# Performance work log

Measured on AMD Instinct MI355X. Metric: run time of the kernel, lower is better.

## Reference

```python
import jax, jax.numpy as jnp
import numpy as np

B, L, D, A = 4, 4096, 256, 64  # batch, seq_len, n_embd, att_size

def setup_inputs() -> dict:
    key = jax.random.key(0)
    kx, kq, kk, kv = jax.random.split(key, 4)
    x = jax.random.normal(kx, (B, L, D), dtype=jnp.float32)
    # torch nn.Linear(n_embd, att_size) weight is [att_size, n_embd]; we store transposed [D, A]
    s = 1.0 / np.sqrt(D)
    Wq = jax.random.normal(kq, (D, A), dtype=jnp.float32) * s
    Wk = jax.random.normal(kk, (D, A), dtype=jnp.float32) * s
    Wv = jax.random.normal(kv, (D, A), dtype=jnp.float32) * s
    return {"x": x, "Wq": Wq, "Wk": Wk, "Wv": Wv}

def reference(x, Wq, Wk, Wv):
    # q,k,v: [B,L,A]
    q = jnp.einsum('bld,da->bla', x, Wq)
    k = jnp.einsum('bld,da->bla', x, Wk)
    v = jnp.einsum('bld,da->bla', x, Wv)
    # NOTE: original module does NOT scale by 1/sqrt(att_size)
    scores = jnp.einsum('bqa,bka->bqk', q, k)  # [B,L,L]
    Lq = x.shape[1]
    causal = jnp.tril(jnp.ones((Lq, Lq), dtype=bool))
    scores = jnp.where(causal, scores, -jnp.inf)
    weights = jax.nn.softmax(scores, axis=-1)
    # dropout is identity in eval mode
    out = jnp.einsum('bqk,bka->bqa', weights, v)  # [B,L,A]
    return out
```

## Files before the change

### kernel.cpp

```cpp
#include <hip/hip_runtime.h>
#include <math.h>

#define B_ 4
#define L_ 4096
#define D_ 256
#define A_ 64
#define M_ (B_*L_)

typedef _Float16 half4 __attribute__((ext_vector_type(4)));
typedef _Float16 half8 __attribute__((ext_vector_type(8)));
typedef __attribute__((ext_vector_type(4))) float floatx4;

__device__ __forceinline__ unsigned short f2h_(float f) {
    _Float16 h = (_Float16)f;
    return __builtin_bit_cast(unsigned short, h);
}

__global__ __launch_bounds__(256) void wconv_kernel(
    const float* __restrict__ Wq, const float* __restrict__ Wk,
    const float* __restrict__ Wv, unsigned short* __restrict__ wt)
{
    const int w = blockIdx.x, t = threadIdx.x;
    const float* W = (w == 0) ? Wq : (w == 1) ? Wk : Wv;
    unsigned short* o = wt + w * A_ * D_;
    const float scale = (w == 0) ? 1.44269504f : 1.0f;
    __shared__ float T[A_ * 260];
    #pragma unroll
    for (int p = 0; p < 16; ++p) {
        int idx = p * 256 + t;
        int d = idx >> 4, a4 = (idx & 15) * 4;
        float4 v = *(const float4*)(W + d * A_ + a4);
        T[(a4 + 0) * 260 + d] = v.x * scale;
        T[(a4 + 1) * 260 + d] = v.y * scale;
        T[(a4 + 2) * 260 + d] = v.z * scale;
        T[(a4 + 3) * 260 + d] = v.w * scale;
    }
    __syncthreads();
    const int a = t >> 2, d0 = (t & 3) * 64;
    #pragma unroll
    for (int i = 0; i < 16; ++i) {
        float4 v = *(const float4*)(&T[a * 260 + d0 + 4 * i]);
        ushort4 s;
        s.x = f2h_(v.x); s.y = f2h_(v.y); s.z = f2h_(v.z); s.w = f2h_(v.w);
        *(ushort4*)(o + a * D_ + d0 + 4 * i) = s;
    }
}

__global__ __launch_bounds__(384) void proj_kernel(
    const float* __restrict__ x,
    const unsigned short* __restrict__ wt,
    unsigned short* __restrict__ qo,
    unsigned short* __restrict__ ko,
    unsigned short* __restrict__ vto)
{
    __shared__ __align__(16) unsigned short Xh[32 * 264];
    __shared__ __align__(16) unsigned short Cst[6 * 1536];
    const int t = threadIdx.x, m0 = blockIdx.x * 32;

    #pragma unroll
    for (int p = 0; p < 6; ++p) {
        int idx = p * 384 + t;
        if (idx < 2048) {
            int row = idx >> 6, col = (idx & 63) * 4;
            float4 v = *(const float4*)(x + (size_t)(m0 + row) * D_ + col);
            ushort4 s;
            s.x = f2h_(v.x); s.y = f2h_(v.y); s.z = f2h_(v.z); s.w = f2h_(v.w);
            *(ushort4*)(Xh + row * 264 + col) = s;
        }
    }
    __syncthreads();

    const int wid = t >> 6, lane = t & 63, c = lane & 15, g = lane >> 4;
    const int w = wid >> 1, mt = wid & 1;

    half8 xa[8];
    #pragma unroll
    for (int s = 0; s < 8; ++s)
        xa[s] = *(const half8*)(Xh + (16 * mt + c) * 264 + 32 * s + 8 * g);

    const unsigned short* wsrc = wt + w * A_ * D_;
    unsigned short* Cw = Cst + wid * 1536;
    #pragma unroll
    for (int nt = 0; nt < 4; ++nt) {
        floatx4 acc = {0.f, 0.f, 0.f, 0.f};
        #pragma unroll
        for (int s = 0; s < 8; ++s) {
            half8 wb = *(const half8*)(wsrc + (16 * nt + c) * D_ + 32 * s + 8 * g);
            acc = __builtin_amdgcn_mfma_f32_16x16x32_f16(xa[s], wb, acc, 0, 0, 0);
        }
        if (w < 2) {
            #pragma unroll
            for (int r = 0; r < 4; ++r)
                Cw[(4 * g + r) * 72 + 16 * nt + c] = f2h_(acc[r]);
        } else {
            #pragma unroll
            for (int r = 0; r < 4; ++r)
                Cw[(16 * nt + c) * 24 + 4 * g + r] = f2h_(acc[r]);
        }
    }

    if (w < 2) {
        unsigned short* o = (w == 0) ? qo : ko;
        const int row16 = lane >> 2, seg = lane & 3;
        uint4 d0 = *(const uint4*)(Cw + row16 * 72 + seg * 16);
        uint4 d1 = *(const uint4*)(Cw + row16 * 72 + seg * 16 + 8);
        unsigned short* p = o + (size_t)(m0 + 16 * mt + row16) * A_ + seg * 16;
        *(uint4*)(p) = d0;
        *(uint4*)(p + 8) = d1;
    }
    __syncthreads();
    if (t < 256) {
        const int a = t >> 2, quarter = t & 3;
        const int o = quarter * 8, mtv = o >> 4, idx = o & 15;
        uint4 d = *(const uint4*)(Cst + (4 + mtv) * 1536 + a * 24 + idx);
        const int bb = m0 >> 12, l0 = m0 & (L_ - 1);
        *(uint4*)(vto + ((size_t)(bb * A_ + a)) * L_ + l0 + o) = d;
    }
}

__global__ __launch_bounds__(256) void attn_kernel(
    const unsigned short* __restrict__ qb,
    const unsigned short* __restrict__ kb,
    const unsigned short* __restrict__ vt,
    float* __restrict__ out,
    float* __restrict__ po1,
    float2* __restrict__ ml0,
    float2* __restrict__ ml1)
{
    __shared__ __align__(16) unsigned short smem[4 * 4608];
    unsigned short* Ks = smem;
    unsigned short* Vs = smem + 2 * 4608;

    const int t    = threadIdx.x;
    const int lane = t & 63;
    const int wid  = t >> 6;
    const int qsub = wid >> 1;
    const int ph   = wid & 1;
    const int c    = lane & 15;
    const int g    = lane >> 4;
    const int b    = blockIdx.y;
    const int bx   = blockIdx.x;
    const int qt   = 127 - (bx >> 1);
    const int h    = bx & 1;
    const int q0   = qt * 32;
    const int qrow0 = q0 + 16 * qsub;
    const int qme  = qrow0 + c;

    const size_t base  = (size_t)b * L_ * A_;
    const size_t vbase = (size_t)b * A_ * L_;

    half8 qf[2];
    {
        const unsigned short* qp = qb + base + (size_t)(qrow0 + c) * A_ + g * 8;
        qf[0] = *(const half8*)(qp);
        qf[1] = *(const half8*)(qp + 32);
    }

    floatx4 O4[4];
    #pragma unroll
    for (int at = 0; at < 4; ++at) O4[at] = (floatx4){0.f, 0.f, 0.f, 0.f};
    float m_ = -INFINITY, l_ = 0.f;

    const int T   = (q0 >> 6) + 1;
    const int Th  = (T + 1) >> 1;
    const int t0  = h ? Th : 0;
    const int t1  = h ? T : Th;
    const int nIt = (t1 - t0 + 1) >> 1;
    const int Tm1 = T - 1;

    for (int it = 0; it < nIt; ++it) {
        __syncthreads();
        #pragma unroll
        for (int tile = 0; tile < 2; ++tile) {
            const int kts = t0 + 2 * it + tile;
            if (kts < t1) {
                const int k0s = kts << 6;
                #pragma unroll
                for (int i = 0; i < 2; ++i) {
                    const int cid = t + (i << 8);
                    const int row = cid >> 3, c8 = cid & 7;
                    uint4 dK = *(const uint4*)(kb + base + (size_t)k0s * 64 + cid * 8);
                    *(uint4*)(Ks + tile * 4608 + row * 72 + c8 * 8) = dK;
                    uint4 dV = *(const uint4*)(vt + vbase + (size_t)row * L_ + k0s + c8 * 8);
                    *(uint4*)(Vs + tile * 4608 + row * 72 + c8 * 8) = dV;
                }
            }
        }
        __syncthreads();

        const int kt = t0 + 2 * it + ph;
        if (kt >= t1) continue;
        const int k0 = kt << 6;
        const unsigned short* Kw = Ks + ph * 4608;
        const unsigned short* Vw = Vs + ph * 4608;

        floatx4 S4[4];
        #pragma unroll
        for (int nt = 0; nt < 4; ++nt) S4[nt] = (floatx4){0.f, 0.f, 0.f, 0.f};
        #pragma unroll
        for (int s = 0; s < 2; ++s)
            #pragma unroll
            for (int nt = 0; nt < 4; ++nt) {
                half8 kf = *(const half8*)(Kw + (16 * nt + c) * 72 + 32 * s + 8 * g);
                S4[nt] = __builtin_amdgcn_mfma_f32_16x16x32_f16(kf, qf[s], S4[nt], 0, 0, 0);
            }

        if (kt == Tm1) {
            #pragma unroll
            for (int nt = 0; nt < 4; ++nt)
                #pragma unroll
                for (int r = 0; r < 4; ++r)
                    if (k0 + 16 * nt + 4 * g + r > qme) S4[nt][r] = -INFINITY;
        }

        float tm = fmaxf(fmaxf(fmaxf(S4[0][0], S4[0][1]), fmaxf(S4[0][2], S4[0][3])),
                         fmaxf(fmaxf(S4[1][0], S4[1][1]), fmaxf(S4[1][2], S4[1][3])));
        tm = fmaxf(tm, fmaxf(fmaxf(fmaxf(S4[2][0], S4[2][1]), fmaxf(S4[2][2], S4[2][3])),
                             fmaxf(fmaxf(S4[3][0], S4[3][1]), fmaxf(S4[3][2], S4[3][3]))));
        tm = fmaxf(tm, __shfl_xor(tm, 16));
        tm = fmaxf(tm, __shfl_xor(tm, 32));
        const float mn  = fmaxf(m_, tm);
        const float mnc = fmaxf(mn, -3.0e38f);
        const float al  = exp2f(fminf(m_ - mnc, 0.f));
        float rs = 0.f;
        half4 pf[4];
        #pragma unroll
        for (int nt = 0; nt < 4; ++nt) {
            #pragma unroll
            for (int r = 0; r < 4; ++r) {
                float p = exp2f(S4[nt][r] - mnc);
                S4[nt][r] = p;
                rs += p;
            }
            pf[nt][0] = (_Float16)S4[nt][0];
            pf[nt][1] = (_Float16)S4[nt][1];
            pf[nt][2] = (_Float16)S4[nt][2];
            pf[nt][3] = (_Float16)S4[nt][3];
        }
        rs += __shfl_xor(rs, 16);
        rs += __shfl_xor(rs, 32);
        l_ = l_ * al + rs;
        m_ = mn;

        #pragma unroll
        for (int at = 0; at < 4; ++at) {
            O4[at] *= al;
            #pragma unroll
            for (int nt = 0; nt < 4; ++nt) {
                half4 va = *(const half4*)(Vw + (16 * at + c) * 72 + 16 * nt + 4 * g);
                O4[at] = __builtin_amdgcn_mfma_f32_16x16x16f16(va, pf[nt], O4[at], 0, 0, 0);
            }
        }
    }

    __syncthreads();
    float*  Of  = (float*)smem;
    float2* mlb = (float2*)(smem + 8192);
    #pragma unroll
    for (int at = 0; at < 4; ++at) {
        float4 v; v.x = O4[at][0]; v.y = O4[at][1]; v.z = O4[at][2]; v.w = O4[at][3];
        ((float4*)Of)[wid * 256 + at * 64 + lane] = v;
    }
    if (g == 0) { float2 ml; ml.x = m_; ml.y = l_; mlb[wid * 16 + c] = ml; }
    __syncthreads();

    {
        const int q32 = t >> 3, seg = t & 7;
        const int qs = q32 >> 4, cc = q32 & 15;
        const float2 A0 = mlb[(2 * qs) * 16 + cc];
        const float2 A1 = mlb[(2 * qs + 1) * 16 + cc];
        const float mf = fmaxf(A0.x, A1.x);
        const float mc = fmaxf(mf, -3.0e38f);
        const float w0 = exp2f(A0.x - mc);
        const float w1 = exp2f(A1.x - mc);
        const float ls = w0 * A0.y + w1 * A1.y;
        float res[8];
        #pragma unroll
        for (int u = 0; u < 8; ++u) {
            const int a = seg * 8 + u;
            const int at = a >> 4, gg = (a >> 2) & 3, r = a & 3;
            const int i0 = ((2 * qs) * 256 + at * 64 + gg * 16 + cc) * 4 + r;
            const int i1 = ((2 * qs + 1) * 256 + at * 64 + gg * 16 + cc) * 4 + r;
            res[u] = w0 * Of[i0] + w1 * Of[i1];
        }
        float* PO = h ? po1 : out;
        float* p = PO + (base + (size_t)(q0 + q32) * A_) + seg * 8;
        *(float4*)(p)     = make_float4(res[0], res[1], res[2], res[3]);
        *(float4*)(p + 4) = make_float4(res[4], res[5], res[6], res[7]);
        if (seg == 0) {
            float2 ml; ml.x = mf; ml.y = ls;
            (h ? ml1 : ml0)[b * L_ + q0 + q32] = ml;
        }
    }
}

__global__ __launch_bounds__(256) void merge_kernel(
    float* __restrict__ out, const float* __restrict__ po1,
    const float2* __restrict__ ml0, const float2* __restrict__ ml1)
{
    const int tg = blockIdx.x * 256 + threadIdx.x;
    const int q = tg >> 4;
    const float2 a0 = ml0[q], a1 = ml1[q];
    const float mf = fmaxf(a0.x, a1.x);
    const float mc = fmaxf(mf, -3.0e38f);
    const float w0 = exp2f(a0.x - mc);
    const float w1 = exp2f(a1.x - mc);
    const float inv = 1.f / (w0 * a0.y + w1 * a1.y);
    float4 o0 = ((const float4*)out)[tg];
    float4 o1 = ((const float4*)po1)[tg];
    float4 r;
    r.x = (o0.x * w0 + o1.x * w1) * inv;
    r.y = (o0.y * w0 + o1.y * w1) * inv;
    r.z = (o0.z * w0 + o1.z * w1) * inv;
    r.w = (o0.w * w0 + o1.w * w1) * inv;
    ((float4*)out)[tg] = r;
}

extern "C" void kernel_launch(void* const* d_in, const int* in_sizes, int n_in,
                              void* d_out, int out_size, void* d_ws, size_t ws_size,
                              hipStream_t stream) {
    const float* x  = (const float*)d_in[0];
    const float* Wq = (const float*)d_in[1];
    const float* Wk = (const float*)d_in[2];
    const float* Wv = (const float*)d_in[3];

    char* ws = (char*)d_ws;
    unsigned short* qb = (unsigned short*)(ws);
    unsigned short* kb = (unsigned short*)(ws + (2u << 20));
    unsigned short* vt = (unsigned short*)(ws + (4u << 20));
    unsigned short* wt = (unsigned short*)(ws + (6u << 20));
    float*  po1 = (float*) (ws + (6u << 20) + 98304);
    float2* ml0 = (float2*)(ws + (6u << 20) + 98304 + (4u << 20));
    float2* ml1 = (float2*)(ws + (6u << 20) + 98304 + (4u << 20) + 131072);
    float* out = (float*)d_out;

    hipLaunchKernelGGL(wconv_kernel, dim3(3), dim3(256), 0, stream, Wq, Wk, Wv, wt);
    hipLaunchKernelGGL(proj_kernel, dim3(M_ / 32), dim3(384), 0, stream, x, wt, qb, kb, vt);
    hipLaunchKernelGGL(attn_kernel, dim3(256, B_), dim3(256), 0, stream,
                       qb, kb, vt, out, po1, ml0, ml1);
    hipLaunchKernelGGL(merge_kernel, dim3(1024), dim3(256), 0, stream, out, po1, ml0, ml1);
}
```

Baseline: 138.1 us.

## Restructure attention into 8-wave blocks with paired q-tiles and fused split-K merge

The attention kernel now runs 512 threads per block, with four waves splitting key tiles for each 16-row query group. Each block processes a heavy and a light causal query tile (127-bx and bx) to balance load. The combine across waves happens in shared memory, which removes the separate merge kernel and the partial-output buffers in the workspace. K tiles are prefetched into registers and written to LDS after a barrier. V fragments are loaded straight from global memory into registers with one tile of lookahead instead of being staged in LDS. The grid shrinks to 256 blocks, and the heavier per-thread V register use may limit occupancy.

After: 198.2 us. 1.44x slower.

```diff
diff --git a/kernel.cpp b/kernel.cpp
--- a/kernel.cpp
+++ b/kernel.cpp
@@ -118,202 +118,199 @@
     }
 }
 
-__global__ __launch_bounds__(256) void attn_kernel(
+__global__ __launch_bounds__(512, 2) void attn_kernel(
     const unsigned short* __restrict__ qb,
     const unsigned short* __restrict__ kb,
     const unsigned short* __restrict__ vt,
-    float* __restrict__ out,
-    float* __restrict__ po1,
-    float2* __restrict__ ml0,
-    float2* __restrict__ ml1)
+    float* __restrict__ out)
 {
     __shared__ __align__(16) unsigned short smem[4 * 4608];
-    unsigned short* Ks = smem;
-    unsigned short* Vs = smem + 2 * 4608;
 
     const int t    = threadIdx.x;
     const int lane = t & 63;
     const int wid  = t >> 6;
-    const int qsub = wid >> 1;
-    const int ph   = wid & 1;
+    const int qsub = wid >> 2;
+    const int ph   = wid & 3;
     const int c    = lane & 15;
     const int g    = lane >> 4;
     const int b    = blockIdx.y;
     const int bx   = blockIdx.x;
-    const int qt   = 127 - (bx >> 1);
-    const int h    = bx & 1;
-    const int q0   = qt * 32;
-    const int qrow0 = q0 + 16 * qsub;
-    const int qme  = qrow0 + c;
 
     const size_t base  = (size_t)b * L_ * A_;
     const size_t vbase = (size_t)b * A_ * L_;
 
-    half8 qf[2];
-    {
-        const unsigned short* qp = qb + base + (size_t)(qrow0 + c) * A_ + g * 8;
-        qf[0] = *(const half8*)(qp);
-        qf[1] = *(const half8*)(qp + 32);
-    }
-
-    floatx4 O4[4];
-    #pragma unroll
-    for (int at = 0; at < 4; ++at) O4[at] = (floatx4){0.f, 0.f, 0.f, 0.f};
-    float m_ = -INFINITY, l_ = 0.f;
-
-    const int T   = (q0 >> 6) + 1;
-    const int Th  = (T + 1) >> 1;
-    const int t0  = h ? Th : 0;
-    const int t1  = h ? T : Th;
-    const int nIt = (t1 - t0 + 1) >> 1;
-    const int Tm1 = T - 1;
-
-    for (int it = 0; it < nIt; ++it) {
+    const int srow = t >> 3, sc8 = t & 7;
+
+    for (int p = 0; p < 2; ++p) {
+        const int qt = (p == 0) ? (127 - bx) : bx;
+        const int q0 = qt * 32;
+        const int qrow0 = q0 + 16 * qsub;
+        const int qme = qrow0 + c;
+        const int T = (qt >> 1) + 1;
+        const int nR = (T + 3) >> 2;
+
+        half8 qf[2];
+        {
+            const unsigned short* qp = qb + base + (size_t)(qrow0 + c) * A_ + g * 8;
+            qf[0] = *(const half8*)(qp);
+            qf[1] = *(const half8*)(qp + 32);
+        }
+
+        floatx4 O4[4];
+        #pragma unroll
+        for (int at = 0; at < 4; ++at) O4[at] = (floatx4){0.f, 0.f, 0.f, 0.f};
+        float m_ = -INFINITY, l_ = 0.f;
+
         __syncthreads();
         #pragma unroll
-        for (int tile = 0; tile < 2; ++tile) {
-            const int kts = t0 + 2 * it + tile;
-            if (kts < t1) {
-                const int k0s = kts << 6;
-                #pragma unroll
-                for (int i = 0; i < 2; ++i) {
-                    const int cid = t + (i << 8);
-                    const int row = cid >> 3, c8 = cid & 7;
-                    uint4 dK = *(const uint4*)(kb + base + (size_t)k0s * 64 + cid * 8);
-                    *(uint4*)(Ks + tile * 4608 + row * 72 + c8 * 8) = dK;
-                    uint4 dV = *(const uint4*)(vt + vbase + (size_t)row * L_ + k0s + c8 * 8);
-                    *(uint4*)(Vs + tile * 4608 + row * 72 + c8 * 8) = dV;
-                }
-            }
-        }
-        __syncthreads();
-
-        const int kt = t0 + 2 * it + ph;
-        if (kt >= t1) continue;
-        const int k0 = kt << 6;
-        const unsigned short* Kw = Ks + ph * 4608;
-        const unsigned short* Vw = Vs + ph * 4608;
-
-        floatx4 S4[4];
-        #pragma unroll
-        for (int nt = 0; nt < 4; ++nt) S4[nt] = (floatx4){0.f, 0.f, 0.f, 0.f};
-        #pragma unroll
-        for (int s = 0; s < 2; ++s)
+        for (int u = 0; u < 4; ++u) {
+            if (u < T) {
+                uint4 dK = *(const uint4*)(kb + base + ((size_t)(u << 6) * 64 + t * 8));
+                *(uint4*)(smem + u * 4608 + srow * 72 + sc8 * 8) = dK;
+            }
+        }
+        half4 vc[4][4], vn[4][4];
+        if (ph < T) {
+            const unsigned short* vp = vt + vbase + (ph << 6);
             #pragma unroll
-            for (int nt = 0; nt < 4; ++nt) {
-                half8 kf = *(const half8*)(Kw + (16 * nt + c) * 72 + 32 * s + 8 * g);
-                S4[nt] = __builtin_amdgcn_mfma_f32_16x16x32_f16(kf, qf[s], S4[nt], 0, 0, 0);
-            }
-
-        if (kt == Tm1) {
-            #pragma unroll
-            for (int nt = 0; nt < 4; ++nt)
-                #pragma unroll
-                for (int r = 0; r < 4; ++r)
-                    if (k0 + 16 * nt + 4 * g + r > qme) S4[nt][r] = -INFINITY;
-        }
-
-        float tm = fmaxf(fmaxf(fmaxf(S4[0][0], S4[0][1]), fmaxf(S4[0][2], S4[0][3])),
-                         fmaxf(fmaxf(S4[1][0], S4[1][1]), fmaxf(S4[1][2], S4[1][3])));
-        tm = fmaxf(tm, fmaxf(fmaxf(fmaxf(S4[2][0], S4[2][1]), fmaxf(S4[2][2], S4[2][3])),
-                             fmaxf(fmaxf(S4[3][0], S4[3][1]), fmaxf(S4[3][2], S4[3][3]))));
-        tm = fmaxf(tm, __shfl_xor(tm, 16));
-        tm = fmaxf(tm, __shfl_xor(tm, 32));
-        const float mn  = fmaxf(m_, tm);
-        const float mnc = fmaxf(mn, -3.0e38f);
-        const float al  = exp2f(fminf(m_ - mnc, 0.f));
-        float rs = 0.f;
-        half4 pf[4];
-        #pragma unroll
-        for (int nt = 0; nt < 4; ++nt) {
-            #pragma unroll
-            for (int r = 0; r < 4; ++r) {
-                float p = exp2f(S4[nt][r] - mnc);
-                S4[nt][r] = p;
-                rs += p;
-            }
-            pf[nt][0] = (_Float16)S4[nt][0];
-            pf[nt][1] = (_Float16)S4[nt][1];
-            pf[nt][2] = (_Float16)S4[nt][2];
-            pf[nt][3] = (_Float16)S4[nt][3];
-        }
-        rs += __shfl_xor(rs, 16);
-        rs += __shfl_xor(rs, 32);
-        l_ = l_ * al + rs;
-        m_ = mn;
-
+            for (int at = 0; at < 4; ++at)
+                #pragma unroll
+                for (int nt = 0; nt < 4; ++nt)
+                    vc[at][nt] = *(const half4*)(vp + (size_t)(16 * at + c) * L_ + 16 * nt + 4 * g);
+        }
+
+        for (int it = 0; it < nR; ++it) {
+            __syncthreads();
+            const int kt = 4 * it + ph;
+            const bool pfk = (it + 1 < nR);
+            uint4 nK[4];
+            if (pfk) {
+                #pragma unroll
+                for (int u = 0; u < 4; ++u) {
+                    const int kts = 4 * (it + 1) + u;
+                    if (kts < T)
+                        nK[u] = *(const uint4*)(kb + base + ((size_t)(kts << 6) * 64 + t * 8));
+                }
+            }
+            if (kt + 4 < T) {
+                const unsigned short* vp = vt + vbase + ((kt + 4) << 6);
+                #pragma unroll
+                for (int at = 0; at < 4; ++at)
+                    #pragma unroll
+                    for (int nt = 0; nt < 4; ++nt)
+                        vn[at][nt] = *(const half4*)(vp + (size_t)(16 * at + c) * L_ + 16 * nt + 4 * g);
+            }
+
+            if (kt < T) {
+                const int k0 = kt << 6;
+                const unsigned short* Kw = smem + ph * 4608;
+
+                floatx4 S4[4];
+                #pragma unroll
+                for (int nt = 0; nt < 4; ++nt) S4[nt] = (floatx4){0.f, 0.f, 0.f, 0.f};
+                #pragma unroll
+                for (int s = 0; s < 2; ++s)
+                    #pragma unroll
+                    for (int nt = 0; nt < 4; ++nt) {
+                        half8 kf = *(const half8*)(Kw + (16 * nt + c) * 72 + 32 * s + 8 * g);
+                        S4[nt] = __builtin_amdgcn_mfma_f32_16x16x32_f16(kf, qf[s], S4[nt], 0, 0, 0);
+                    }
+
+                if (kt == T - 1) {
+                    #pragma unroll
+                    for (int nt = 0; nt < 4; ++nt)
+                        #pragma unroll
+                        for (int r = 0; r < 4; ++r)
+                            if (k0 + 16 * nt + 4 * g + r > qme) S4[nt][r] = -INFINITY;
+                }
+
+                float tm = fmaxf(fmaxf(fmaxf(S4[0][0], S4[0][1]), fmaxf(S4[0][2], S4[0][3])),
+                                 fmaxf(fmaxf(S4[1][0], S4[1][1]), fmaxf(S4[1][2], S4[1][3])));
+                tm = fmaxf(tm, fmaxf(fmaxf(fmaxf(S4[2][0], S4[2][1]), fmaxf(S4[2][2], S4[2][3])),
+                                     fmaxf(fmaxf(S4[3][0], S4[3][1]), fmaxf(S4[3][2], S4[3][3]))));
+                tm = fmaxf(tm, __shfl_xor(tm, 16));
+                tm = fmaxf(tm, __shfl_xor(tm, 32));
+                const float mn  = fmaxf(m_, tm);
+                const float mnc = fmaxf(mn, -3.0e38f);
+                const float al  = exp2f(fminf(m_ - mnc, 0.f));
+                float rs = 0.f;
+                half4 pfr[4];
+                #pragma unroll
+                for (int nt = 0; nt < 4; ++nt) {
+                    #pragma unroll
+                    for (int r = 0; r < 4; ++r) {
+                        float pv = exp2f(S4[nt][r] - mnc);
+                        S4[nt][r] = pv;
+                        rs += pv;
+                    }
+                    pfr[nt][0] = (_Float16)S4[nt][0];
+                    pfr[nt][1] = (_Float16)S4[nt][1];
+                    pfr[nt][2] = (_Float16)S4[nt][2];
+                    pfr[nt][3] = (_Float16)S4[nt][3];
+                }
+                rs += __shfl_xor(rs, 16);
+                rs += __shfl_xor(rs, 32);
+                l_ = l_ * al + rs;
+                m_ = mn;
+
+                #pragma unroll
+                for (int at = 0; at < 4; ++at) {
+                    O4[at] *= al;
+                    #pragma unroll
+                    for (int nt = 0; nt < 4; ++nt)
+                        O4[at] = __builtin_amdgcn_mfma_f32_16x16x16f16(vc[at][nt], pfr[nt], O4[at], 0, 0, 0);
+                }
+                if (kt + 4 < T) {
+                    #pragma unroll
+                    for (int at = 0; at < 4; ++at)
+                        #pragma unroll
+                        for (int nt = 0; nt < 4; ++nt)
+                            vc[at][nt] = vn[at][nt];
+                }
+            }
+
+            __syncthreads();
+            if (pfk) {
+                #pragma unroll
+                for (int u = 0; u < 4; ++u)
+                    if (4 * (it + 1) + u < T)
+                        *(uint4*)(smem + u * 4608 + srow * 72 + sc8 * 8) = nK[u];
+            }
+        }
+
+        float4* Obuf = (float4*)smem;
+        float2* mlq  = (float2*)((char*)smem + 32768);
         #pragma unroll
         for (int at = 0; at < 4; ++at) {
-            O4[at] *= al;
-            #pragma unroll
-            for (int nt = 0; nt < 4; ++nt) {
-                half4 va = *(const half4*)(Vw + (16 * at + c) * 72 + 16 * nt + 4 * g);
-                O4[at] = __builtin_amdgcn_mfma_f32_16x16x16f16(va, pf[nt], O4[at], 0, 0, 0);
-            }
-        }
-    }
-
-    __syncthreads();
-    float*  Of  = (float*)smem;
-    float2* mlb = (float2*)(smem + 8192);
-    #pragma unroll
-    for (int at = 0; at < 4; ++at) {
-        float4 v; v.x = O4[at][0]; v.y = O4[at][1]; v.z = O4[at][2]; v.w = O4[at][3];
-        ((float4*)Of)[wid * 256 + at * 64 + lane] = v;
-    }
-    if (g == 0) { float2 ml; ml.x = m_; ml.y = l_; mlb[wid * 16 + c] = ml; }
-    __syncthreads();
-
-    {
-        const int q32 = t >> 3, seg = t & 7;
-        const int qs = q32 >> 4, cc = q32 & 15;
-        const float2 A0 = mlb[(2 * qs) * 16 + cc];
-        const float2 A1 = mlb[(2 * qs + 1) * 16 + cc];
-        const float mf = fmaxf(A0.x, A1.x);
-        const float mc = fmaxf(mf, -3.0e38f);
-        const float w0 = exp2f(A0.x - mc);
-        const float w1 = exp2f(A1.x - mc);
-        const float ls = w0 * A0.y + w1 * A1.y;
-        float res[8];
-        #pragma unroll
-        for (int u = 0; u < 8; ++u) {
-            const int a = seg * 8 + u;
-            const int at = a >> 4, gg = (a >> 2) & 3, r = a & 3;
-            const int i0 = ((2 * qs) * 256 + at * 64 + gg * 16 + cc) * 4 + r;
-            const int i1 = ((2 * qs + 1) * 256 + at * 64 + gg * 16 + cc) * 4 + r;
-            res[u] = w0 * Of[i0] + w1 * Of[i1];
-        }
-        float* PO = h ? po1 : out;
-        float* p = PO + (base + (size_t)(q0 + q32) * A_) + seg * 8;
-        *(float4*)(p)     = make_float4(res[0], res[1], res[2], res[3]);
-        *(float4*)(p + 4) = make_float4(res[4], res[5], res[6], res[7]);
-        if (seg == 0) {
-            float2 ml; ml.x = mf; ml.y = ls;
-            (h ? ml1 : ml0)[b * L_ + q0 + q32] = ml;
-        }
-    }
-}
-
-__global__ __launch_bounds__(256) void merge_kernel(
-    float* __restrict__ out, const float* __restrict__ po1,
-    const float2* __restrict__ ml0, const float2* __restrict__ ml1)
-{
-    const int tg = blockIdx.x * 256 + threadIdx.x;
-    const int q = tg >> 4;
-    const float2 a0 = ml0[q], a1 = ml1[q];
-    const float mf = fmaxf(a0.x, a1.x);
-    const float mc = fmaxf(mf, -3.0e38f);
-    const float w0 = exp2f(a0.x - mc);
-    const float w1 = exp2f(a1.x - mc);
-    const float inv = 1.f / (w0 * a0.y + w1 * a1.y);
-    float4 o0 = ((const float4*)out)[tg];
-    float4 o1 = ((const float4*)po1)[tg];
-    float4 r;
-    r.x = (o0.x * w0 + o1.x * w1) * inv;
-    r.y = (o0.y * w0 + o1.y * w1) * inv;
-    r.z = (o0.z * w0 + o1.z * w1) * inv;
-    r.w = (o0.w * w0 + o1.w * w1) * inv;
-    ((float4*)out)[tg] = r;
+            float4 v; v.x = O4[at][0]; v.y = O4[at][1]; v.z = O4[at][2]; v.w = O4[at][3];
+            Obuf[wid * 256 + at * 64 + lane] = v;
+        }
+        if (g == 0) { float2 ml; ml.x = m_; ml.y = l_; mlq[wid * 16 + c] = ml; }
+        __syncthreads();
+        {
+            const int q = t >> 4, seg = t & 15;
+            const int qs = q >> 4, cc = q & 15;
+            const int at = seg >> 2, gg = seg & 3;
+            const float2 A0 = mlq[(qs * 4 + 0) * 16 + cc];
+            const float2 A1 = mlq[(qs * 4 + 1) * 16 + cc];
+            const float2 A2 = mlq[(qs * 4 + 2) * 16 + cc];
+            const float2 A3 = mlq[(qs * 4 + 3) * 16 + cc];
+            const float mf = fmaxf(fmaxf(A0.x, A1.x), fmaxf(A2.x, A3.x));
+            const float w0 = exp2f(A0.x - mf), w1 = exp2f(A1.x - mf);
+            const float w2 = exp2f(A2.x - mf), w3 = exp2f(A3.x - mf);
+            const float inv = 1.f / (w0 * A0.y + w1 * A1.y + w2 * A2.y + w3 * A3.y);
+            const float4 o0 = Obuf[(qs * 4 + 0) * 256 + at * 64 + gg * 16 + cc];
+            const float4 o1 = Obuf[(qs * 4 + 1) * 256 + at * 64 + gg * 16 + cc];
+            const float4 o2 = Obuf[(qs * 4 + 2) * 256 + at * 64 + gg * 16 + cc];
+            const float4 o3 = Obuf[(qs * 4 + 3) * 256 + at * 64 + gg * 16 + cc];
+            float4 r;
+            r.x = (o0.x * w0 + o1.x * w1 + o2.x * w2 + o3.x * w3) * inv;
+            r.y = (o0.y * w0 + o1.y * w1 + o2.y * w2 + o3.y * w3) * inv;
+            r.z = (o0.z * w0 + o1.z * w1 + o2.z * w2 + o3.z * w3) * inv;
+            r.w = (o0.w * w0 + o1.w * w1 + o2.w * w2 + o3.w * w3) * inv;
+            *(float4*)(out + base + (size_t)(q0 + q) * A_ + seg * 4) = r;
+        }
+    }
 }
 
 extern "C" void kernel_launch(void* const* d_in, const int* in_sizes, int n_in,
@@ -329,14 +326,9 @@
     unsigned short* kb = (unsigned short*)(ws + (2u << 20));
     unsigned short* vt = (unsigned short*)(ws + (4u << 20));
     unsigned short* wt = (unsigned short*)(ws + (6u << 20));
-    float*  po1 = (float*) (ws + (6u << 20) + 98304);
-    float2* ml0 = (float2*)(ws + (6u << 20) + 98304 + (4u << 20));
-    float2* ml1 = (float2*)(ws + (6u << 20) + 98304 + (4u << 20) + 131072);
     float* out = (float*)d_out;
 
     hipLaunchKernelGGL(wconv_kernel, dim3(3), dim3(256), 0, stream, Wq, Wk, Wv, wt);
     hipLaunchKernelGGL(proj_kernel, dim3(M_ / 32), dim3(384), 0, stream, x, wt, qb, kb, vt);
-    hipLaunchKernelGGL(attn_kernel, dim3(256, B_), dim3(256), 0, stream,
-                       qb, kb, vt, out, po1, ml0, ml1);
-    hipLaunchKernelGGL(merge_kernel, dim3(1024), dim3(256), 0, stream, out, po1, ml0, ml1);
-}
+    hipLaunchKernelGGL(attn_kernel, dim3(64, B_), dim3(512), 0, stream, qb, kb, vt, out);
+}
```

## Have each attention wave process both query subtiles to reuse K/V fragments

Applied to the files above, without the earlier changes.

The attention block shrinks from four waves to two, and each wave now handles both 16-row query subtiles of the 32-row tile. Each K and V fragment read from LDS then feeds two MFMAs, which halves LDS read traffic per unit of compute and cuts the number of waves sharing the staged tiles. In exchange, per-wave register use roughly doubles (two sets of accumulators and scores), fewer threads share the global-to-LDS copy, and there are fewer waves available to hide latency. The in-block combine and the workspace offsets are adjusted to match.

New measurement: 141.9 us. 1.03x slower.

```diff
diff --git a/kernel.cpp b/kernel.cpp
--- a/kernel.cpp
+++ b/kernel.cpp
@@ -118,7 +118,7 @@
     }
 }
 
-__global__ __launch_bounds__(256) void attn_kernel(
+__global__ __launch_bounds__(128) void attn_kernel(
     const unsigned short* __restrict__ qb,
     const unsigned short* __restrict__ kb,
     const unsigned short* __restrict__ vt,
@@ -133,9 +133,7 @@
 
     const int t    = threadIdx.x;
     const int lane = t & 63;
-    const int wid  = t >> 6;
-    const int qsub = wid >> 1;
-    const int ph   = wid & 1;
+    const int ph   = t >> 6;
     const int c    = lane & 15;
     const int g    = lane >> 4;
     const int b    = blockIdx.y;
@@ -143,25 +141,28 @@
     const int qt   = 127 - (bx >> 1);
     const int h    = bx & 1;
     const int q0   = qt * 32;
-    const int qrow0 = q0 + 16 * qsub;
-    const int qme  = qrow0 + c;
 
     const size_t base  = (size_t)b * L_ * A_;
     const size_t vbase = (size_t)b * A_ * L_;
 
-    half8 qf[2];
-    {
-        const unsigned short* qp = qb + base + (size_t)(qrow0 + c) * A_ + g * 8;
-        qf[0] = *(const half8*)(qp);
-        qf[1] = *(const half8*)(qp + 32);
-    }
-
-    floatx4 O4[4];
-    #pragma unroll
-    for (int at = 0; at < 4; ++at) O4[at] = (floatx4){0.f, 0.f, 0.f, 0.f};
-    float m_ = -INFINITY, l_ = 0.f;
-
-    const int T   = (q0 >> 6) + 1;
+    half8 qf[2][2];
+    #pragma unroll
+    for (int u = 0; u < 2; ++u) {
+        const unsigned short* qp = qb + base + (size_t)(q0 + 16 * u + c) * A_ + g * 8;
+        qf[u][0] = *(const half8*)(qp);
+        qf[u][1] = *(const half8*)(qp + 32);
+    }
+
+    floatx4 O4[2][4];
+    float m_[2], l_[2];
+    #pragma unroll
+    for (int u = 0; u < 2; ++u) {
+        #pragma unroll
+        for (int at = 0; at < 4; ++at) O4[u][at] = (floatx4){0.f, 0.f, 0.f, 0.f};
+        m_[u] = -INFINITY; l_[u] = 0.f;
+    }
+
+    const int T   = (qt >> 1) + 1;
     const int Th  = (T + 1) >> 1;
     const int t0  = h ? Th : 0;
     const int t1  = h ? T : Th;
@@ -176,8 +177,8 @@
             if (kts < t1) {
                 const int k0s = kts << 6;
                 #pragma unroll
-                for (int i = 0; i < 2; ++i) {
-                    const int cid = t + (i << 8);
+                for (int i = 0; i < 4; ++i) {
+                    const int cid = t + (i << 7);
                     const int row = cid >> 3, c8 = cid & 7;
                     uint4 dK = *(const uint4*)(kb + base + (size_t)k0s * 64 + cid * 8);
                     *(uint4*)(Ks + tile * 4608 + row * 72 + c8 * 8) = dK;
@@ -194,102 +195,118 @@
         const unsigned short* Kw = Ks + ph * 4608;
         const unsigned short* Vw = Vs + ph * 4608;
 
-        floatx4 S4[4];
-        #pragma unroll
-        for (int nt = 0; nt < 4; ++nt) S4[nt] = (floatx4){0.f, 0.f, 0.f, 0.f};
+        floatx4 S4[2][4];
+        #pragma unroll
+        for (int u = 0; u < 2; ++u)
+            #pragma unroll
+            for (int nt = 0; nt < 4; ++nt) S4[u][nt] = (floatx4){0.f, 0.f, 0.f, 0.f};
         #pragma unroll
         for (int s = 0; s < 2; ++s)
             #pragma unroll
             for (int nt = 0; nt < 4; ++nt) {
                 half8 kf = *(const half8*)(Kw + (16 * nt + c) * 72 + 32 * s + 8 * g);
-                S4[nt] = __builtin_amdgcn_mfma_f32_16x16x32_f16(kf, qf[s], S4[nt], 0, 0, 0);
+                S4[0][nt] = __builtin_amdgcn_mfma_f32_16x16x32_f16(kf, qf[0][s], S4[0][nt], 0, 0, 0);
+                S4[1][nt] = __builtin_amdgcn_mfma_f32_16x16x32_f16(kf, qf[1][s], S4[1][nt], 0, 0, 0);
             }
 
         if (kt == Tm1) {
             #pragma unroll
-            for (int nt = 0; nt < 4; ++nt)
+            for (int u = 0; u < 2; ++u) {
+                const int qme = q0 + 16 * u + c;
                 #pragma unroll
-                for (int r = 0; r < 4; ++r)
-                    if (k0 + 16 * nt + 4 * g + r > qme) S4[nt][r] = -INFINITY;
-        }
-
-        float tm = fmaxf(fmaxf(fmaxf(S4[0][0], S4[0][1]), fmaxf(S4[0][2], S4[0][3])),
-                         fmaxf(fmaxf(S4[1][0], S4[1][1]), fmaxf(S4[1][2], S4[1][3])));
-        tm = fmaxf(tm, fmaxf(fmaxf(fmaxf(S4[2][0], S4[2][1]), fmaxf(S4[2][2], S4[2][3])),
-                             fmaxf(fmaxf(S4[3][0], S4[3][1]), fmaxf(S4[3][2], S4[3][3]))));
-        tm = fmaxf(tm, __shfl_xor(tm, 16));
-        tm = fmaxf(tm, __shfl_xor(tm, 32));
-        const float mn  = fmaxf(m_, tm);
-        const float mnc = fmaxf(mn, -3.0e38f);
-        const float al  = exp2f(fminf(m_ - mnc, 0.f));
-        float rs = 0.f;
-        half4 pf[4];
-        #pragma unroll
-        for (int nt = 0; nt < 4; ++nt) {
-            #pragma unroll
-            for (int r = 0; r < 4; ++r) {
-                float p = exp2f(S4[nt][r] - mnc);
-                S4[nt][r] = p;
-                rs += p;
-            }
-            pf[nt][0] = (_Float16)S4[nt][0];
-            pf[nt][1] = (_Float16)S4[nt][1];
-            pf[nt][2] = (_Float16)S4[nt][2];
-            pf[nt][3] = (_Float16)S4[nt][3];
-        }
-        rs += __shfl_xor(rs, 16);
-        rs += __shfl_xor(rs, 32);
-        l_ = l_ * al + rs;
-        m_ = mn;
+                for (int nt = 0; nt < 4; ++nt)
+                    #pragma unroll
+                    for (int r = 0; r < 4; ++r)
+                        if (k0 + 16 * nt + 4 * g + r > qme) S4[u][nt][r] = -INFINITY;
+            }
+        }
+
+        half4 pfr[2][4];
+        float al[2];
+        #pragma unroll
+        for (int u = 0; u < 2; ++u) {
+            float tm = fmaxf(fmaxf(fmaxf(S4[u][0][0], S4[u][0][1]), fmaxf(S4[u][0][2], S4[u][0][3])),
+                             fmaxf(fmaxf(S4[u][1][0], S4[u][1][1]), fmaxf(S4[u][1][2], S4[u][1][3])));
+            tm = fmaxf(tm, fmaxf(fmaxf(fmaxf(S4[u][2][0], S4[u][2][1]), fmaxf(S4[u][2][2], S4[u][2][3])),
+                                 fmaxf(fmaxf(S4[u][3][0], S4[u][3][1]), fmaxf(S4[u][3][2], S4[u][3][3]))));
+            tm = fmaxf(tm, __shfl_xor(tm, 16));
+            tm = fmaxf(tm, __shfl_xor(tm, 32));
+            const float mn  = fmaxf(m_[u], tm);
+            const float mnc = fmaxf(mn, -3.0e38f);
+            al[u] = exp2f(fminf(m_[u] - mnc, 0.f));
+            float rs = 0.f;
+            #pragma unroll
+            for (int nt = 0; nt < 4; ++nt) {
+                #pragma unroll
+                for (int r = 0; r < 4; ++r) {
+                    float pv = exp2f(S4[u][nt][r] - mnc);
+                    S4[u][nt][r] = pv;
+                    rs += pv;
+                }
+                pfr[u][nt][0] = (_Float16)S4[u][nt][0];
+                pfr[u][nt][1] = (_Float16)S4[u][nt][1];
+                pfr[u][nt][2] = (_Float16)S4[u][nt][2];
+                pfr[u][nt][3] = (_Float16)S4[u][nt][3];
+            }
+            rs += __shfl_xor(rs, 16);
+            rs += __shfl_xor(rs, 32);
+            l_[u] = l_[u] * al[u] + rs;
+            m_[u] = mn;
+        }
 
         #pragma unroll
         for (int at = 0; at < 4; ++at) {
-            O4[at] *= al;
+            O4[0][at] *= al[0];
+            O4[1][at] *= al[1];
             #pragma unroll
             for (int nt = 0; nt < 4; ++nt) {
                 half4 va = *(const half4*)(Vw + (16 * at + c) * 72 + 16 * nt + 4 * g);
-                O4[at] = __builtin_amdgcn_mfma_f32_16x16x16f16(va, pf[nt], O4[at], 0, 0, 0);
-            }
-        }
-    }
-
-    __syncthreads();
-    float*  Of  = (float*)smem;
-    float2* mlb = (float2*)(smem + 8192);
-    #pragma unroll
-    for (int at = 0; at < 4; ++at) {
-        float4 v; v.x = O4[at][0]; v.y = O4[at][1]; v.z = O4[at][2]; v.w = O4[at][3];
-        ((float4*)Of)[wid * 256 + at * 64 + lane] = v;
-    }
-    if (g == 0) { float2 ml; ml.x = m_; ml.y = l_; mlb[wid * 16 + c] = ml; }
-    __syncthreads();
-
+                O4[0][at] = __builtin_amdgcn_mfma_f32_16x16x16f16(va, pfr[0][nt], O4[0][at], 0, 0, 0);
+                O4[1][at] = __builtin_amdgcn_mfma_f32_16x16x16f16(va, pfr[1][nt], O4[1][at], 0, 0, 0);
+            }
+        }
+    }
+
+    __syncthreads();
+    float4* Obuf = (float4*)smem;
+    float2* mlq  = (float2*)((char*)smem + 16384);
+    #pragma unroll
+    for (int u = 0; u < 2; ++u) {
+        #pragma unroll
+        for (int at = 0; at < 4; ++at) {
+            float4 v; v.x = O4[u][at][0]; v.y = O4[u][at][1];
+            v.z = O4[u][at][2]; v.w = O4[u][at][3];
+            Obuf[((ph * 2 + u) * 4 + at) * 64 + lane] = v;
+        }
+        if (g == 0) { float2 ml; ml.x = m_[u]; ml.y = l_[u]; mlq[(ph * 2 + u) * 16 + c] = ml; }
+    }
+    __syncthreads();
     {
-        const int q32 = t >> 3, seg = t & 7;
-        const int qs = q32 >> 4, cc = q32 & 15;
-        const float2 A0 = mlb[(2 * qs) * 16 + cc];
-        const float2 A1 = mlb[(2 * qs + 1) * 16 + cc];
+        const int q = t >> 2, seg = t & 3;
+        const int u = q >> 4, cc = q & 15;
+        const float2 A0 = mlq[(0 * 2 + u) * 16 + cc];
+        const float2 A1 = mlq[(1 * 2 + u) * 16 + cc];
         const float mf = fmaxf(A0.x, A1.x);
         const float mc = fmaxf(mf, -3.0e38f);
         const float w0 = exp2f(A0.x - mc);
         const float w1 = exp2f(A1.x - mc);
         const float ls = w0 * A0.y + w1 * A1.y;
-        float res[8];
-        #pragma unroll
-        for (int u = 0; u < 8; ++u) {
-            const int a = seg * 8 + u;
-            const int at = a >> 4, gg = (a >> 2) & 3, r = a & 3;
-            const int i0 = ((2 * qs) * 256 + at * 64 + gg * 16 + cc) * 4 + r;
-            const int i1 = ((2 * qs + 1) * 256 + at * 64 + gg * 16 + cc) * 4 + r;
-            res[u] = w0 * Of[i0] + w1 * Of[i1];
+        float res[16];
+        #pragma unroll
+        for (int j = 0; j < 16; ++j) {
+            const int gg = j >> 2, r = j & 3;
+            const float* e0 = (const float*)&Obuf[((0 * 2 + u) * 4 + seg) * 64 + gg * 16 + cc];
+            const float* e1 = (const float*)&Obuf[((1 * 2 + u) * 4 + seg) * 64 + gg * 16 + cc];
+            res[j] = w0 * e0[r] + w1 * e1[r];
         }
         float* PO = h ? po1 : out;
-        float* p = PO + (base + (size_t)(q0 + q32) * A_) + seg * 8;
-        *(float4*)(p)     = make_float4(res[0], res[1], res[2], res[3]);
-        *(float4*)(p + 4) = make_float4(res[4], res[5], res[6], res[7]);
+        float* p = PO + base + (size_t)(q0 + q) * A_ + seg * 16;
+        #pragma unroll
+        for (int v = 0; v < 4; ++v)
+            *(float4*)(p + 4 * v) = make_float4(res[4*v], res[4*v+1], res[4*v+2], res[4*v+3]);
         if (seg == 0) {
             float2 ml; ml.x = mf; ml.y = ls;
-            (h ? ml1 : ml0)[b * L_ + q0 + q32] = ml;
+            (h ? ml1 : ml0)[b * L_ + q0 + q] = ml;
         }
     }
 }
@@ -329,14 +346,14 @@
     unsigned short* kb = (unsigned short*)(ws + (2u << 20));
     unsigned short* vt = (unsigned short*)(ws + (4u << 20));
     unsigned short* wt = (unsigned short*)(ws + (6u << 20));
-    float*  po1 = (float*) (ws + (6u << 20) + 98304);
-    float2* ml0 = (float2*)(ws + (6u << 20) + 98304 + (4u << 20));
-    float2* ml1 = (float2*)(ws + (6u << 20) + 98304 + (4u << 20) + 131072);
+    float*  po1 = (float*) (ws + (6u << 20) + (128u << 10));
+    float2* ml0 = (float2*)(ws + (10u << 20) + (128u << 10));
+    float2* ml1 = (float2*)(ws + (10u << 20) + (256u << 10));
     float* out = (float*)d_out;
 
     hipLaunchKernelGGL(wconv_kernel, dim3(3), dim3(256), 0, stream, Wq, Wk, Wv, wt);
     hipLaunchKernelGGL(proj_kernel, dim3(M_ / 32), dim3(384), 0, stream, x, wt, qb, kb, vt);
-    hipLaunchKernelGGL(attn_kernel, dim3(256, B_), dim3(256), 0, stream,
+    hipLaunchKernelGGL(attn_kernel, dim3(256, B_), dim3(128), 0, stream,
                        qb, kb, vt, out, po1, ml0, ml1);
     hipLaunchKernelGGL(merge_kernel, dim3(1024), dim3(256), 0, stream, out, po1, ml0, ml1);
 }
```

## Split causal attention KV range into fixed 512-key chunks with fp16 partials

Applied to the files above, without the earlier changes.

Replaces the two-way split of each query tile's key range with up to eight splits of eight 64-key tiles each. Splits beyond what a query tile needs exit early, which evens out per-block work under the causal mask and raises parallelism. Non-first partial outputs are stored in fp16 in a packed buffer to reduce workspace traffic, and the merge kernel combines a variable number of splits. The risks are many empty launched blocks, extra merge reads, and some precision loss from the fp16 partials.

Measured after the change: 166.5 us. 1.21x slower.

```diff
diff --git a/kernel.cpp b/kernel.cpp
--- a/kernel.cpp
+++ b/kernel.cpp
@@ -15,6 +15,12 @@
     _Float16 h = (_Float16)f;
     return __builtin_bit_cast(unsigned short, h);
 }
+__device__ __forceinline__ float h2f_(unsigned short u) {
+    return (float)__builtin_bit_cast(_Float16, u);
+}
+
+__device__ __constant__ int c_poff[8] =
+    {0, 0, 917504, 1703936, 2359296, 2883584, 3276800, 3538944};
 
 __global__ __launch_bounds__(256) void wconv_kernel(
     const float* __restrict__ Wq, const float* __restrict__ Wk,
@@ -123,9 +129,8 @@
     const unsigned short* __restrict__ kb,
     const unsigned short* __restrict__ vt,
     float* __restrict__ out,
-    float* __restrict__ po1,
-    float2* __restrict__ ml0,
-    float2* __restrict__ ml1)
+    unsigned short* __restrict__ pack,
+    float2* __restrict__ mls)
 {
     __shared__ __align__(16) unsigned short smem[4 * 4608];
     unsigned short* Ks = smem;
@@ -138,13 +143,17 @@
     const int ph   = wid & 1;
     const int c    = lane & 15;
     const int g    = lane >> 4;
-    const int b    = blockIdx.y;
-    const int bx   = blockIdx.x;
-    const int qt   = 127 - (bx >> 1);
-    const int h    = bx & 1;
+    const int s    = blockIdx.x & 7;
+    const int b    = blockIdx.x >> 3;
+    const int qt   = 127 - blockIdx.y;
     const int q0   = qt * 32;
+
+    const int T  = (qt >> 1) + 1;
+    const int ns = (T + 7) >> 3;
+    if (s >= ns) return;
+
     const int qrow0 = q0 + 16 * qsub;
-    const int qme  = qrow0 + c;
+    const int qme   = qrow0 + c;
 
     const size_t base  = (size_t)b * L_ * A_;
     const size_t vbase = (size_t)b * A_ * L_;
@@ -161,10 +170,8 @@
     for (int at = 0; at < 4; ++at) O4[at] = (floatx4){0.f, 0.f, 0.f, 0.f};
     float m_ = -INFINITY, l_ = 0.f;
 
-    const int T   = (q0 >> 6) + 1;
-    const int Th  = (T + 1) >> 1;
-    const int t0  = h ? Th : 0;
-    const int t1  = h ? T : Th;
+    const int t0  = 8 * s;
+    const int t1  = min(T, t0 + 8);
     const int nIt = (t1 - t0 + 1) >> 1;
     const int Tm1 = T - 1;
 
@@ -198,11 +205,11 @@
         #pragma unroll
         for (int nt = 0; nt < 4; ++nt) S4[nt] = (floatx4){0.f, 0.f, 0.f, 0.f};
         #pragma unroll
-        for (int s = 0; s < 2; ++s)
+        for (int ss = 0; ss < 2; ++ss)
             #pragma unroll
             for (int nt = 0; nt < 4; ++nt) {
-                half8 kf = *(const half8*)(Kw + (16 * nt + c) * 72 + 32 * s + 8 * g);
-                S4[nt] = __builtin_amdgcn_mfma_f32_16x16x32_f16(kf, qf[s], S4[nt], 0, 0, 0);
+                half8 kf = *(const half8*)(Kw + (16 * nt + c) * 72 + 32 * ss + 8 * g);
+                S4[nt] = __builtin_amdgcn_mfma_f32_16x16x32_f16(kf, qf[ss], S4[nt], 0, 0, 0);
             }
 
         if (kt == Tm1) {
@@ -223,19 +230,19 @@
         const float mnc = fmaxf(mn, -3.0e38f);
         const float al  = exp2f(fminf(m_ - mnc, 0.f));
         float rs = 0.f;
-        half4 pf[4];
+        half4 pfr[4];
         #pragma unroll
         for (int nt = 0; nt < 4; ++nt) {
             #pragma unroll
             for (int r = 0; r < 4; ++r) {
-                float p = exp2f(S4[nt][r] - mnc);
-                S4[nt][r] = p;
-                rs += p;
+                float pv = exp2f(S4[nt][r] - mnc);
+                S4[nt][r] = pv;
+                rs += pv;
             }
-            pf[nt][0] = (_Float16)S4[nt][0];
-            pf[nt][1] = (_Float16)S4[nt][1];
-            pf[nt][2] = (_Float16)S4[nt][2];
-            pf[nt][3] = (_Float16)S4[nt][3];
+            pfr[nt][0] = (_Float16)S4[nt][0];
+            pfr[nt][1] = (_Float16)S4[nt][1];
+            pfr[nt][2] = (_Float16)S4[nt][2];
+            pfr[nt][3] = (_Float16)S4[nt][3];
         }
         rs += __shfl_xor(rs, 16);
         rs += __shfl_xor(rs, 32);
@@ -248,27 +255,27 @@
             #pragma unroll
             for (int nt = 0; nt < 4; ++nt) {
                 half4 va = *(const half4*)(Vw + (16 * at + c) * 72 + 16 * nt + 4 * g);
-                O4[at] = __builtin_amdgcn_mfma_f32_16x16x16f16(va, pf[nt], O4[at], 0, 0, 0);
+                O4[at] = __builtin_amdgcn_mfma_f32_16x16x16f16(va, pfr[nt], O4[at], 0, 0, 0);
             }
         }
     }
 
     __syncthreads();
     float*  Of  = (float*)smem;
-    float2* mlb = (float2*)(smem + 8192);
+    float2* mlq = (float2*)(smem + 8192);
     #pragma unroll
     for (int at = 0; at < 4; ++at) {
         float4 v; v.x = O4[at][0]; v.y = O4[at][1]; v.z = O4[at][2]; v.w = O4[at][3];
         ((float4*)Of)[wid * 256 + at * 64 + lane] = v;
     }
-    if (g == 0) { float2 ml; ml.x = m_; ml.y = l_; mlb[wid * 16 + c] = ml; }
+    if (g == 0) { float2 ml; ml.x = m_; ml.y = l_; mlq[wid * 16 + c] = ml; }
     __syncthreads();
 
     {
         const int q32 = t >> 3, seg = t & 7;
         const int qs = q32 >> 4, cc = q32 & 15;
-        const float2 A0 = mlb[(2 * qs) * 16 + cc];
-        const float2 A1 = mlb[(2 * qs + 1) * 16 + cc];
+        const float2 A0 = mlq[(2 * qs) * 16 + cc];
+        const float2 A1 = mlq[(2 * qs + 1) * 16 + cc];
         const float mf = fmaxf(A0.x, A1.x);
         const float mc = fmaxf(mf, -3.0e38f);
         const float w0 = exp2f(A0.x - mc);
@@ -283,37 +290,65 @@
             const int i1 = ((2 * qs + 1) * 256 + at * 64 + gg * 16 + cc) * 4 + r;
             res[u] = w0 * Of[i0] + w1 * Of[i1];
         }
-        float* PO = h ? po1 : out;
-        float* p = PO + (base + (size_t)(q0 + q32) * A_) + seg * 8;
-        *(float4*)(p)     = make_float4(res[0], res[1], res[2], res[3]);
-        *(float4*)(p + 4) = make_float4(res[4], res[5], res[6], res[7]);
+        const int l = q0 + q32;
+        if (s == 0) {
+            float* p = out + base + (size_t)l * A_ + seg * 8;
+            *(float4*)(p)     = make_float4(res[0], res[1], res[2], res[3]);
+            *(float4*)(p + 4) = make_float4(res[4], res[5], res[6], res[7]);
+        } else {
+            const int rows_s = 4096 - 512 * s;
+            unsigned short* p = pack + c_poff[s]
+                + (((size_t)(b * rows_s + (l - 512 * s))) << 6) + seg * 8;
+            ushort4 u0, u1;
+            u0.x = f2h_(res[0]); u0.y = f2h_(res[1]); u0.z = f2h_(res[2]); u0.w = f2h_(res[3]);
+            u1.x = f2h_(res[4]); u1.y = f2h_(res[5]); u1.z = f2h_(res[6]); u1.w = f2h_(res[7]);
+            *(ushort4*)(p)     = u0;
+            *(ushort4*)(p + 4) = u1;
+        }
         if (seg == 0) {
             float2 ml; ml.x = mf; ml.y = ls;
-            (h ? ml1 : ml0)[b * L_ + q0 + q32] = ml;
+            mls[(size_t)s * M_ + b * L_ + l] = ml;
         }
     }
 }
 
 __global__ __launch_bounds__(256) void merge_kernel(
-    float* __restrict__ out, const float* __restrict__ po1,
-    const float2* __restrict__ ml0, const float2* __restrict__ ml1)
+    float* __restrict__ out, const unsigned short* __restrict__ pack,
+    const float2* __restrict__ mls)
 {
-    const int tg = blockIdx.x * 256 + threadIdx.x;
-    const int q = tg >> 4;
-    const float2 a0 = ml0[q], a1 = ml1[q];
-    const float mf = fmaxf(a0.x, a1.x);
-    const float mc = fmaxf(mf, -3.0e38f);
-    const float w0 = exp2f(a0.x - mc);
-    const float w1 = exp2f(a1.x - mc);
-    const float inv = 1.f / (w0 * a0.y + w1 * a1.y);
-    float4 o0 = ((const float4*)out)[tg];
-    float4 o1 = ((const float4*)po1)[tg];
-    float4 r;
-    r.x = (o0.x * w0 + o1.x * w1) * inv;
-    r.y = (o0.y * w0 + o1.y * w1) * inv;
-    r.z = (o0.z * w0 + o1.z * w1) * inv;
-    r.w = (o0.w * w0 + o1.w * w1) * inv;
-    ((float4*)out)[tg] = r;
+    const int tid = blockIdx.x * 256 + threadIdx.x;
+    const int q = tid >> 2, seg = tid & 3;
+    const int l = q & (L_ - 1), b = q >> 12;
+    const int qt = l >> 5;
+    const int T  = (qt >> 1) + 1;
+    const int ns = (T + 7) >> 3;
+
+    float2 a[8];
+    a[0] = mls[q];
+    float mf = a[0].x;
+    for (int s = 1; s < ns; ++s) { a[s] = mls[(size_t)s * M_ + q]; mf = fmaxf(mf, a[s].x); }
+    float w[8], lsum = 0.f;
+    for (int s = 0; s < ns; ++s) { w[s] = exp2f(a[s].x - mf); lsum += w[s] * a[s].y; }
+    const float inv = 1.f / lsum;
+
+    float acc[16];
+    {
+        const float* p = out + (size_t)q * A_ + seg * 16;
+        #pragma unroll
+        for (int u = 0; u < 16; ++u) acc[u] = w[0] * p[u];
+    }
+    for (int s = 1; s < ns; ++s) {
+        const int rows_s = 4096 - 512 * s;
+        const unsigned short* p = pack + c_poff[s]
+            + (((size_t)(b * rows_s + (l - 512 * s))) << 6) + seg * 16;
+        #pragma unroll
+        for (int u = 0; u < 16; ++u) acc[u] += w[s] * h2f_(p[u]);
+    }
+    float* o = out + (size_t)q * A_ + seg * 16;
+    #pragma unroll
+    for (int u = 0; u < 4; ++u)
+        *(float4*)(o + 4 * u) = make_float4(acc[4*u] * inv, acc[4*u+1] * inv,
+                                            acc[4*u+2] * inv, acc[4*u+3] * inv);
 }
 
 extern "C" void kernel_launch(void* const* d_in, const int* in_sizes, int n_in,
@@ -325,18 +360,17 @@
     const float* Wv = (const float*)d_in[3];
 
     char* ws = (char*)d_ws;
-    unsigned short* qb = (unsigned short*)(ws);
-    unsigned short* kb = (unsigned short*)(ws + (2u << 20));
-    unsigned short* vt = (unsigned short*)(ws + (4u << 20));
-    unsigned short* wt = (unsigned short*)(ws + (6u << 20));
-    float*  po1 = (float*) (ws + (6u << 20) + 98304);
-    float2* ml0 = (float2*)(ws + (6u << 20) + 98304 + (4u << 20));
-    float2* ml1 = (float2*)(ws + (6u << 20) + 98304 + (4u << 20) + 131072);
+    unsigned short* qb   = (unsigned short*)(ws);
+    unsigned short* kb   = (unsigned short*)(ws + (2u << 20));
+    unsigned short* vt   = (unsigned short*)(ws + (4u << 20));
+    unsigned short* wt   = (unsigned short*)(ws + (6u << 20));
+    unsigned short* pack = (unsigned short*)(ws + (6u << 20) + 131072);
+    float2*         mls  = (float2*)(ws + (6u << 20) + 131072 + 7340032);
     float* out = (float*)d_out;
 
     hipLaunchKernelGGL(wconv_kernel, dim3(3), dim3(256), 0, stream, Wq, Wk, Wv, wt);
     hipLaunchKernelGGL(proj_kernel, dim3(M_ / 32), dim3(384), 0, stream, x, wt, qb, kb, vt);
-    hipLaunchKernelGGL(attn_kernel, dim3(256, B_), dim3(256), 0, stream,
-                       qb, kb, vt, out, po1, ml0, ml1);
-    hipLaunchKernelGGL(merge_kernel, dim3(1024), dim3(256), 0, stream, out, po1, ml0, ml1);
-}
+    hipLaunchKernelGGL(attn_kernel, dim3(32, 128), dim3(256), 0, stream,
+                       qb, kb, vt, out, pack, mls);
+    hipLaunchKernelGGL(merge_kernel, dim3(256), dim3(256), 0, stream, out, pack, mls);
+}
```
